# Optimization experiments

Hardware: AMD Instinct MI355X
Metric: run time of the kernel (lower is better)

The kernel has to match this reference:

```python
import jax, jax.numpy as jnp
import numpy as np

EPS = 1e-5  # BatchNorm eps (torch default)

def _bn(x, gamma, beta):
    # training-mode BatchNorm over the edge/node (leading) axis, biased var
    mean = x.mean(axis=0, keepdims=True)
    var = x.var(axis=0, keepdims=True)
    return (x - mean) * jax.lax.rsqrt(var + EPS) * gamma + beta

def _silu(x):
    return x * jax.nn.sigmoid(x)

def setup_inputs() -> dict:
    N, E, H, NH = 50000, 800000, 128, 4
    HD = H // NH
    key = jax.random.key(0)
    ks = jax.random.split(key, 8)
    x = jax.random.normal(ks[0], (N, H), dtype=jnp.float32)
    weight = jax.random.uniform(ks[1], (N, 1), dtype=jnp.float32)  # positive fraction weights
    src = jax.random.randint(ks[2], (E,), 0, N)
    dst = jax.random.randint(ks[3], (E,), 0, N)
    # f: Linear(2H, 1) + BN(1)
    Wf = jax.random.normal(ks[4], (2 * H, 1), dtype=jnp.float32) * 0.05
    bf = jnp.zeros((1,), jnp.float32)
    f_gamma = jnp.ones((1,), jnp.float32)
    f_beta = jnp.zeros((1,), jnp.float32)
    # g: NH heads of Linear(2H, HD) + BN(HD), stacked on leading head axis
    Wg = jax.random.normal(ks[5], (NH, 2 * H, HD), dtype=jnp.float32) * 0.05
    bg = jnp.zeros((NH, HD), jnp.float32)
    g_gamma = jnp.ones((NH, HD), jnp.float32)
    g_beta = jnp.zeros((NH, HD), jnp.float32)
    # bn_nodes: BN(H)
    n_gamma = jnp.ones((H,), jnp.float32)
    n_beta = jnp.zeros((H,), jnp.float32)
    return dict(x=x, weight=weight, src=src, dst=dst, Wf=Wf, bf=bf,
                f_gamma=f_gamma, f_beta=f_beta, Wg=Wg, bg=bg,
                g_gamma=g_gamma, g_beta=g_beta, n_gamma=n_gamma, n_beta=n_beta)

def reference(x, weight, src, dst, Wf, bf, f_gamma, f_beta, Wg, bg, g_gamma, g_beta, n_gamma, n_beta):
    N = x.shape[0]
    E = src.shape[0]
    # per-edge concat of src/dst node features: [E, 2H]
    hihj = jnp.concatenate([x[src], x[dst]], axis=-1)
    # attention logit f(hihj) = SiLU(BN(Linear)) then exp: [E, 1]
    exp_e = jnp.exp(_silu(_bn(hihj @ Wf + bf, f_gamma, f_beta)))
    # weighted softmax-like normalization over incoming edges of each dst node
    we = weight[src] * exp_e                                   # [E, 1]
    sum_w_exp = jax.ops.segment_sum(we, dst, num_segments=N)   # [N, 1]
    a = we / sum_w_exp[dst]                                    # [E, 1]
    # multi-head message: a_ij * SiLU(BN(Linear_h(hihj))) per head, concat
    z = jnp.einsum('ed,hdk->ehk', hihj, Wg) + bg               # [E, NH, HD]
    z = _silu(_bn(z, g_gamma, g_beta))
    msg = (a[:, :, None] * z).reshape(E, -1)                   # [E, H]
    h = jax.ops.segment_sum(msg, dst, num_segments=N)          # [N, H]
    out = _bn(h, n_gamma, n_beta) + x                          # residual
    return out
```

## Files before the change

kernel.cpp:

```cpp
#include <hip/hip_runtime.h>
#include <hip/hip_bf16.h>
#include <math.h>

#define HDIM 128
#define PAD 64
typedef unsigned short ushort_t;
typedef unsigned int uint_t;
typedef __attribute__((ext_vector_type(8))) short bf16x8;
typedef __attribute__((ext_vector_type(4))) float f32x4;
typedef __attribute__((ext_vector_type(2))) float v2f;

__device__ __forceinline__ float wave_allreduce(float v){
  #pragma unroll
  for (int o = 1; o < 64; o <<= 1) v += __shfl_xor(v, o);
  return v;
}

__device__ __forceinline__ ushort_t f2bf(float f){
  uint_t u = __float_as_uint(f);
  uint_t r = (u + 0x7fffu + ((u >> 16) & 1u)) >> 16;
  return (ushort_t)r;
}

__device__ __forceinline__ v2f bf2(uint_t u){
  v2f r;
  r.x = __uint_as_float(u << 16);
  r.y = __uint_as_float(u & 0xffff0000u);
  return r;
}

__global__ __launch_bounds__(128) void k_wpack(const float* __restrict__ Wg,
    const float* __restrict__ Wf, ushort_t* __restrict__ W2t,
    int* __restrict__ cnt, int N){
  int b = blockIdx.x;
  int k = threadIdx.x;
  if (b < 272){
    float val;
    if (b < 128)       val = Wg[(size_t)(b >> 5) * 8192 + k * 32 + (b & 31)];
    else if (b < 256){ int c2 = b - 128;
                       val = Wg[(size_t)(c2 >> 5) * 8192 + (k + 128) * 32 + (c2 & 31)]; }
    else if (b == 256) val = Wf[k];
    else if (b == 257) val = Wf[128 + k];
    else               val = 0.f;
    W2t[(size_t)b * 128 + k] = f2bf(val);
  } else {
    int i = (b - 272) * 128 + k;
    if (i < N) cnt[i] = 0;
  }
}

__global__ __launch_bounds__(256) void k_gemmfill(const float* __restrict__ x,
    const ushort_t* __restrict__ W2t, const float* __restrict__ weight,
    ushort_t* __restrict__ Pb, ushort_t* __restrict__ Qb,
    float* __restrict__ v, float2* __restrict__ uw2,
    const int* __restrict__ src, const int* __restrict__ dst,
    int* __restrict__ cnt, int* __restrict__ es,
    int N, int E, int GB){
  if ((int)blockIdx.x < GB){
    int wid = __builtin_amdgcn_readfirstlane(threadIdx.x >> 6);
    int lane = threadIdx.x & 63;
    int quad = lane >> 4, col = lane & 15;
    int strip = blockIdx.x * 2 + (wid >> 1);
    int half = wid & 1;
    int n_base = strip * 16;
    if (n_base >= N) return;
    int tbeg = half * 8;
    int ntile = half ? 9 : 8;
    f32x4 acc[9];
    #pragma unroll
    for (int t = 0; t < 9; ++t) acc[t] = (f32x4){0.f, 0.f, 0.f, 0.f};
    int row = n_base + col;
    int rowc = row < N ? row : N - 1;
    const float* xr = x + (size_t)rowc * HDIM + quad * 8;
    #pragma unroll
    for (int kk = 0; kk < 4; ++kk){
      float4 a0 = *(const float4*)(xr + kk * 32);
      float4 a1 = *(const float4*)(xr + kk * 32 + 4);
      bf16x8 af;
      af[0] = (short)f2bf(a0.x); af[1] = (short)f2bf(a0.y);
      af[2] = (short)f2bf(a0.z); af[3] = (short)f2bf(a0.w);
      af[4] = (short)f2bf(a1.x); af[5] = (short)f2bf(a1.y);
      af[6] = (short)f2bf(a1.z); af[7] = (short)f2bf(a1.w);
      const ushort_t* wb = W2t + (size_t)(tbeg * 16) * 128 + (size_t)col * 128 + kk * 32 + quad * 8;
      #pragma unroll
      for (int t = 0; t < 9; ++t){
        if (t < ntile){
          bf16x8 bfr = *(const bf16x8*)(wb + (size_t)t * 16 * 128);
          acc[t] = __builtin_amdgcn_mfma_f32_16x16x32_bf16(af, bfr, acc[t], 0, 0, 0);
        }
      }
    }
    #pragma unroll
    for (int t = 0; t < 8; ++t){
      int ct = tbeg + t;
      int c = ct * 16 + col;
      #pragma unroll
      for (int r = 0; r < 4; ++r){
        int n = n_base + quad * 4 + r;
        if (n < N){
          ushort_t valb = f2bf(acc[t][r]);
          if (c < 128) Pb[(size_t)n * HDIM + c] = valb;
          else         Qb[(size_t)n * HDIM + (c - 128)] = valb;
        }
      }
    }
    if (half){
      #pragma unroll
      for (int r = 0; r < 4; ++r){
        int n = n_base + quad * 4 + r;
        if (n < N){
          float val = acc[8][r];
          if (col == 0)      uw2[n] = make_float2(val, weight[n]);
          else if (col == 1) v[n] = val;
        }
      }
    }
  } else {
    int bi = blockIdx.x - GB;
    int part = bi & 7;
    int nch = (gridDim.x - GB) >> 3;
    int chunk = bi >> 3;
    int Npp = (N + 7) >> 3;
    int lo = part * Npp;
    int hi = lo + Npp; if (hi > N) hi = N;
    int stride = nch * 256;
    for (int e = chunk * 256 + threadIdx.x; e < E; e += stride){
      int d = dst[e];
      if (d >= lo && d < hi){
        int c = atomicAdd(&cnt[d], 1);
        if (c < PAD) es[(size_t)d * PAD + c] = src[e];
      }
    }
  }
}

__global__ __launch_bounds__(256) void k_gstats(const ushort_t* __restrict__ Pb,
    const ushort_t* __restrict__ Qb, const float* __restrict__ v,
    const float2* __restrict__ uw2, const int* __restrict__ es,
    const int* __restrict__ cnt, float* __restrict__ pstatG, int N, int NW){
  int lane = threadIdx.x & 63;
  int wid = __builtin_amdgcn_readfirstlane(threadIdx.x >> 6);
  int wg = blockIdx.x * 4 + wid;
  const uint_t* Pu = (const uint_t*)Pb;
  const uint_t* Qu = (const uint_t*)Qb;
  v2f gs = {0.f, 0.f}, gq = {0.f, 0.f};
  float fs = 0.f, fq = 0.f;
  for (int n = wg; n < N; n += NW){
    int dn = cnt[n]; dn = dn < PAD ? dn : PAD;
    v2f q = bf2(Qu[(size_t)n * 64 + lane]);
    float vn = v[n];
    int sj = 0;
    if (lane < dn){
      sj = es[(size_t)n * PAD + lane];
      float t = uw2[sj].x + vn;
      fs += t; fq = fmaf(t, t, fq);
    }
    int j = 0;
    for (; j + 3 < dn; j += 4){
      int s0 = __shfl(sj, j),     s1 = __shfl(sj, j + 1);
      int s2 = __shfl(sj, j + 2), s3 = __shfl(sj, j + 3);
      uint_t p0 = Pu[(size_t)s0 * 64 + lane];
      uint_t p1 = Pu[(size_t)s1 * 64 + lane];
      uint_t p2 = Pu[(size_t)s2 * 64 + lane];
      uint_t p3 = Pu[(size_t)s3 * 64 + lane];
      v2f y0 = bf2(p0) + q, y1 = bf2(p1) + q, y2 = bf2(p2) + q, y3 = bf2(p3) + q;
      gs += y0 + y1 + y2 + y3;
      gq += y0 * y0; gq += y1 * y1; gq += y2 * y2; gq += y3 * y3;
    }
    for (; j < dn; ++j){
      int s0 = __shfl(sj, j);
      v2f y0 = bf2(Pu[(size_t)s0 * 64 + lane]) + q;
      gs += y0; gq += y0 * y0;
    }
  }
  fs = wave_allreduce(fs); fq = wave_allreduce(fq);
  float* pb = pstatG + (size_t)wg * 258;
  *(float2*)&pb[2 * lane]       = make_float2(gs.x, gs.y);
  *(float2*)&pb[128 + 2 * lane] = make_float2(gq.x, gq.y);
  if (lane == 0){ pb[256] = fs; pb[257] = fq; }
}

__global__ __launch_bounds__(256) void k_redfin1(const float* __restrict__ pstatG,
    int NW, const float* __restrict__ g_gamma, const float* __restrict__ g_beta,
    const float* __restrict__ f_gamma, const float* __restrict__ f_beta,
    float* __restrict__ fin, long long E){
  int j = blockIdx.x;
  int c1 = (j < 128) ? j : 256;
  int c2 = (j < 128) ? 128 + j : 257;
  double s1 = 0, s2 = 0;
  for (int b = threadIdx.x; b < NW; b += 256){
    const float* pb = pstatG + (size_t)b * 258;
    s1 += (double)pb[c1]; s2 += (double)pb[c2];
  }
  __shared__ double m1[256], m2[256];
  m1[threadIdx.x] = s1; m2[threadIdx.x] = s2;
  __syncthreads();
  for (int o = 128; o; o >>= 1){
    if (threadIdx.x < o){ m1[threadIdx.x] += m1[threadIdx.x + o];
                          m2[threadIdx.x] += m2[threadIdx.x + o]; }
    __syncthreads();
  }
  if (threadIdx.x == 0){
    double m = m1[0] / (double)E;
    double var = m2[0] / (double)E - m * m;
    if (j < 128){
      float sc = (float)((double)g_gamma[j] / sqrt(var + 1e-5));
      fin[2 + j] = sc; fin[130 + j] = g_beta[j] - (float)m * sc;
    } else {
      float sc = (float)((double)f_gamma[0] / sqrt(var + 1e-5));
      fin[0] = sc; fin[1] = f_beta[0] - (float)m * sc;
    }
  }
}

__global__ __launch_bounds__(256) void k_msg(const ushort_t* __restrict__ Pb,
    const ushort_t* __restrict__ Qb, const float* __restrict__ v,
    const float2* __restrict__ uw2, const int* __restrict__ es,
    const int* __restrict__ cnt, const float* __restrict__ fin,
    float* __restrict__ h, float* __restrict__ pstatH, int N, int NW){
  int lane = threadIdx.x & 63;
  int wid = __builtin_amdgcn_readfirstlane(threadIdx.x >> 6);
  int wg = blockIdx.x * 4 + wid;
  const uint_t* Pu = (const uint_t*)Pb;
  const uint_t* Qu = (const uint_t*)Qb;
  float fsc = fin[0], fsh = fin[1];
  v2f gsc = {fin[2 + 2 * lane], fin[3 + 2 * lane]};
  v2f gsh = {fin[130 + 2 * lane], fin[131 + 2 * lane]};
  v2f hs = {0.f, 0.f}, hq = {0.f, 0.f};
  for (int n = wg; n < N; n += NW){
    int dn = cnt[n]; dn = dn < PAD ? dn : PAD;
    float vn = v[n];
    int sj = 0; float wj = 0.f;
    if (lane < dn){
      sj = es[(size_t)n * PAD + lane];
      float2 uw = uw2[sj];
      float t = fmaf(uw.x + vn, fsc, fsh);
      float sl = t * __builtin_amdgcn_rcpf(1.f + __expf(-t));
      wj = uw.y * __expf(sl);
    }
    float sw = wave_allreduce(wj);
    wj *= (dn > 0) ? (1.f / sw) : 0.f;
    v2f q = bf2(Qu[(size_t)n * 64 + lane]);
    v2f acc = {0.f, 0.f};
    int j = 0;
    for (; j + 3 < dn; j += 4){
      int s0 = __shfl(sj, j),     s1 = __shfl(sj, j + 1);
      int s2 = __shfl(sj, j + 2), s3 = __shfl(sj, j + 3);
      float a0 = __shfl(wj, j),     a1 = __shfl(wj, j + 1);
      float a2 = __shfl(wj, j + 2), a3 = __shfl(wj, j + 3);
      uint_t p0 = Pu[(size_t)s0 * 64 + lane];
      uint_t p1 = Pu[(size_t)s1 * 64 + lane];
      uint_t p2 = Pu[(size_t)s2 * 64 + lane];
      uint_t p3 = Pu[(size_t)s3 * 64 + lane];
      {
        v2f y = (bf2(p0) + q) * gsc + gsh;
        float e0 = __expf(-y.x), e1 = __expf(-y.y);
        float d0 = 1.f + e0, d1 = 1.f + e1;
        float r = __builtin_amdgcn_rcpf(d0 * d1) * a0;
        v2f z; z.x = y.x * d1; z.y = y.y * d0;
        acc += z * (v2f){r, r};
      }
      {
        v2f y = (bf2(p1) + q) * gsc + gsh;
        float e0 = __expf(-y.x), e1 = __expf(-y.y);
        float d0 = 1.f + e0, d1 = 1.f + e1;
        float r = __builtin_amdgcn_rcpf(d0 * d1) * a1;
        v2f z; z.x = y.x * d1; z.y = y.y * d0;
        acc += z * (v2f){r, r};
      }
      {
        v2f y = (bf2(p2) + q) * gsc + gsh;
        float e0 = __expf(-y.x), e1 = __expf(-y.y);
        float d0 = 1.f + e0, d1 = 1.f + e1;
        float r = __builtin_amdgcn_rcpf(d0 * d1) * a2;
        v2f z; z.x = y.x * d1; z.y = y.y * d0;
        acc += z * (v2f){r, r};
      }
      {
        v2f y = (bf2(p3) + q) * gsc + gsh;
        float e0 = __expf(-y.x), e1 = __expf(-y.y);
        float d0 = 1.f + e0, d1 = 1.f + e1;
        float r = __builtin_amdgcn_rcpf(d0 * d1) * a3;
        v2f z; z.x = y.x * d1; z.y = y.y * d0;
        acc += z * (v2f){r, r};
      }
    }
    for (; j < dn; ++j){
      int s0 = __shfl(sj, j);
      float a0 = __shfl(wj, j);
      v2f y = (bf2(Pu[(size_t)s0 * 64 + lane]) + q) * gsc + gsh;
      float e0 = __expf(-y.x), e1 = __expf(-y.y);
      float d0 = 1.f + e0, d1 = 1.f + e1;
      float r = __builtin_amdgcn_rcpf(d0 * d1) * a0;
      v2f z; z.x = y.x * d1; z.y = y.y * d0;
      acc += z * (v2f){r, r};
    }
    *(float2*)&h[(size_t)n * 128 + 2 * lane] = make_float2(acc.x, acc.y);
    hs += acc; hq += acc * acc;
  }
  float* pb = pstatH + (size_t)wg * 256;
  *(float2*)&pb[2 * lane]       = make_float2(hs.x, hs.y);
  *(float2*)&pb[128 + 2 * lane] = make_float2(hq.x, hq.y);
}

__global__ __launch_bounds__(256) void k_redfin2(const float* __restrict__ pstatH,
    int NW, const float* __restrict__ n_gamma, const float* __restrict__ n_beta,
    float* __restrict__ fin, int N){
  int j = blockIdx.x;
  double s1 = 0, s2 = 0;
  for (int b = threadIdx.x; b < NW; b += 256){
    const float* pb = pstatH + (size_t)b * 256;
    s1 += (double)pb[j]; s2 += (double)pb[128 + j];
  }
  __shared__ double m1[256], m2[256];
  m1[threadIdx.x] = s1; m2[threadIdx.x] = s2;
  __syncthreads();
  for (int o = 128; o; o >>= 1){
    if (threadIdx.x < o){ m1[threadIdx.x] += m1[threadIdx.x + o];
                          m2[threadIdx.x] += m2[threadIdx.x + o]; }
    __syncthreads();
  }
  if (threadIdx.x == 0){
    double m = m1[0] / (double)N;
    double var = m2[0] / (double)N - m * m;
    float sc = (float)((double)n_gamma[j] / sqrt(var + 1e-5));
    fin[258 + j] = sc; fin[386 + j] = n_beta[j] - (float)m * sc;
  }
}

__global__ __launch_bounds__(256) void k_out(const float* __restrict__ h,
    const float* __restrict__ x, const float* __restrict__ fin,
    float* __restrict__ out, int total4){
  int i = blockIdx.x * 256 + threadIdx.x;
  if (i >= total4) return;
  const float4* h4 = (const float4*)h; const float4* x4 = (const float4*)x;
  float4 hv = h4[i], xv = x4[i];
  int c = (i * 4) & 127;
  float4 o;
  o.x = fmaf(hv.x, fin[258 + c],     fin[386 + c])     + xv.x;
  o.y = fmaf(hv.y, fin[258 + c + 1], fin[386 + c + 1]) + xv.y;
  o.z = fmaf(hv.z, fin[258 + c + 2], fin[386 + c + 2]) + xv.z;
  o.w = fmaf(hv.w, fin[258 + c + 3], fin[386 + c + 3]) + xv.w;
  ((float4*)out)[i] = o;
}

extern "C" void kernel_launch(void* const* d_in, const int* in_sizes, int n_in,
                              void* d_out, int out_size, void* d_ws, size_t ws_size,
                              hipStream_t stream){
  const float* x       = (const float*)d_in[0];
  const float* weight  = (const float*)d_in[1];
  const int*   src     = (const int*)d_in[2];
  const int*   dst     = (const int*)d_in[3];
  const float* Wf      = (const float*)d_in[4];
  const float* f_gamma = (const float*)d_in[6];
  const float* f_beta  = (const float*)d_in[7];
  const float* Wg      = (const float*)d_in[8];
  const float* g_gamma = (const float*)d_in[10];
  const float* g_beta  = (const float*)d_in[11];
  const float* n_gamma = (const float*)d_in[12];
  const float* n_beta  = (const float*)d_in[13];
  float* out = (float*)d_out;

  int N = in_sizes[0] / HDIM;
  int E = in_sizes[2];

  char* ws = (char*)d_ws;
  size_t off = 0;
  auto alloc = [&](size_t bytes)->char*{
    char* p = ws + off; off = (off + bytes + 255) & ~(size_t)255; return p;
  };
  ushort_t* Pb    = (ushort_t*)alloc((size_t)N * HDIM * 2);
  ushort_t* Qb    = (ushort_t*)alloc((size_t)N * HDIM * 2);
  float* h        = (float*)alloc((size_t)N * HDIM * 4);
  float* v        = (float*)alloc((size_t)N * 4);
  float2* uw2     = (float2*)alloc((size_t)N * 8);
  int* es         = (int*)alloc((size_t)N * PAD * 4);
  ushort_t* W2t   = (ushort_t*)alloc((size_t)272 * 128 * 2);
  int* cnt        = (int*)alloc((size_t)N * 4);
  const int NWB = 2048;
  const int NW  = NWB * 4;
  float*  pstatG = (float*)alloc((size_t)NW * 258 * 4);
  float*  pstatH = (float*)alloc((size_t)NW * 256 * 4);
  float*  fin    = (float*)alloc(514 * 4);

  int GB = (N + 31) / 32;
  const int FB = 4096;

  k_wpack   <<<272 + (N + 127) / 128, 128, 0, stream>>>(Wg, Wf, W2t, cnt, N);
  k_gemmfill<<<GB + FB, 256, 0, stream>>>(x, W2t, weight, Pb, Qb, v, uw2,
                                          src, dst, cnt, es, N, E, GB);
  k_gstats  <<<NWB, 256, 0, stream>>>(Pb, Qb, v, uw2, es, cnt, pstatG, N, NW);
  k_redfin1 <<<129, 256, 0, stream>>>(pstatG, NW, g_gamma, g_beta, f_gamma, f_beta, fin, (long long)E);
  k_msg     <<<NWB, 256, 0, stream>>>(Pb, Qb, v, uw2, es, cnt, fin, h, pstatH, N, NW);
  k_redfin2 <<<128, 256, 0, stream>>>(pstatH, NW, n_gamma, n_beta, fin, N);
  k_out     <<<(N * HDIM / 4 + 255) / 256, 256, 0, stream>>>(h, x, fin, out, N * HDIM / 4);
}
```

Baseline: 302.2 us.

## Fuse stats, reductions, message and output into one cooperative kernel with grid syncs

Replaces the gstats, redfin1, msg, redfin2 and out kernels with a single cooperative kernel that uses grid.sync() between phases, launched with 1024 blocks (down from 2048 waves-blocks), and splits the combined GEMM/fill kernel into two separate launches. The goal is to remove per-launch overhead and the gaps between the small reduction kernels. In exchange it adds grid-wide barrier cost, limits the grid to co-resident blocks, and serializes the GEMM and edge fill instead of running them concurrently in one launch.

```diff
diff --git a/kernel.cpp b/kernel.cpp
--- a/kernel.cpp
+++ b/kernel.cpp
@@ -1,6 +1,9 @@
 #include <hip/hip_runtime.h>
 #include <hip/hip_bf16.h>
+#include <hip/hip_cooperative_groups.h>
 #include <math.h>
+
+namespace cg = cooperative_groups;
 
 #define HDIM 128
 #define PAD 64
@@ -49,299 +52,297 @@
   }
 }
 
-__global__ __launch_bounds__(256) void k_gemmfill(const float* __restrict__ x,
+__global__ __launch_bounds__(256) void k_gemm2(const float* __restrict__ x,
     const ushort_t* __restrict__ W2t, const float* __restrict__ weight,
     ushort_t* __restrict__ Pb, ushort_t* __restrict__ Qb,
-    float* __restrict__ v, float2* __restrict__ uw2,
-    const int* __restrict__ src, const int* __restrict__ dst,
-    int* __restrict__ cnt, int* __restrict__ es,
-    int N, int E, int GB){
-  if ((int)blockIdx.x < GB){
-    int wid = __builtin_amdgcn_readfirstlane(threadIdx.x >> 6);
-    int lane = threadIdx.x & 63;
-    int quad = lane >> 4, col = lane & 15;
-    int strip = blockIdx.x * 2 + (wid >> 1);
-    int half = wid & 1;
-    int n_base = strip * 16;
-    if (n_base >= N) return;
-    int tbeg = half * 8;
-    int ntile = half ? 9 : 8;
-    f32x4 acc[9];
+    float* __restrict__ v, float2* __restrict__ uw2, int N){
+  int wid = __builtin_amdgcn_readfirstlane(threadIdx.x >> 6);
+  int lane = threadIdx.x & 63;
+  int quad = lane >> 4, col = lane & 15;
+  int strip = blockIdx.x * 2 + (wid >> 1);
+  int half = wid & 1;
+  int n_base = strip * 16;
+  if (n_base >= N) return;
+  int tbeg = half * 8;
+  int ntile = half ? 9 : 8;
+  f32x4 acc[9];
+  #pragma unroll
+  for (int t = 0; t < 9; ++t) acc[t] = (f32x4){0.f, 0.f, 0.f, 0.f};
+  int row = n_base + col;
+  int rowc = row < N ? row : N - 1;
+  const float* xr = x + (size_t)rowc * HDIM + quad * 8;
+  #pragma unroll
+  for (int kk = 0; kk < 4; ++kk){
+    float4 a0 = *(const float4*)(xr + kk * 32);
+    float4 a1 = *(const float4*)(xr + kk * 32 + 4);
+    bf16x8 af;
+    af[0] = (short)f2bf(a0.x); af[1] = (short)f2bf(a0.y);
+    af[2] = (short)f2bf(a0.z); af[3] = (short)f2bf(a0.w);
+    af[4] = (short)f2bf(a1.x); af[5] = (short)f2bf(a1.y);
+    af[6] = (short)f2bf(a1.z); af[7] = (short)f2bf(a1.w);
+    const ushort_t* wb = W2t + (size_t)(tbeg * 16) * 128 + (size_t)col * 128 + kk * 32 + quad * 8;
     #pragma unroll
-    for (int t = 0; t < 9; ++t) acc[t] = (f32x4){0.f, 0.f, 0.f, 0.f};
-    int row = n_base + col;
-    int rowc = row < N ? row : N - 1;
-    const float* xr = x + (size_t)rowc * HDIM + quad * 8;
+    for (int t = 0; t < 9; ++t){
+      if (t < ntile){
+        bf16x8 bfr = *(const bf16x8*)(wb + (size_t)t * 16 * 128);
+        acc[t] = __builtin_amdgcn_mfma_f32_16x16x32_bf16(af, bfr, acc[t], 0, 0, 0);
+      }
+    }
+  }
+  #pragma unroll
+  for (int t = 0; t < 8; ++t){
+    int ct = tbeg + t;
+    int c = ct * 16 + col;
     #pragma unroll
-    for (int kk = 0; kk < 4; ++kk){
-      float4 a0 = *(const float4*)(xr + kk * 32);
-      float4 a1 = *(const float4*)(xr + kk * 32 + 4);
-      bf16x8 af;
-      af[0] = (short)f2bf(a0.x); af[1] = (short)f2bf(a0.y);
-      af[2] = (short)f2bf(a0.z); af[3] = (short)f2bf(a0.w);
-      af[4] = (short)f2bf(a1.x); af[5] = (short)f2bf(a1.y);
-      af[6] = (short)f2bf(a1.z); af[7] = (short)f2bf(a1.w);
-      const ushort_t* wb = W2t + (size_t)(tbeg * 16) * 128 + (size_t)col * 128 + kk * 32 + quad * 8;
-      #pragma unroll
-      for (int t = 0; t < 9; ++t){
-        if (t < ntile){
-          bf16x8 bfr = *(const bf16x8*)(wb + (size_t)t * 16 * 128);
-          acc[t] = __builtin_amdgcn_mfma_f32_16x16x32_bf16(af, bfr, acc[t], 0, 0, 0);
-        }
-      }
-    }
+    for (int r = 0; r < 4; ++r){
+      int n = n_base + quad * 4 + r;
+      if (n < N){
+        ushort_t valb = f2bf(acc[t][r]);
+        if (c < 128) Pb[(size_t)n * HDIM + c] = valb;
+        else         Qb[(size_t)n * HDIM + (c - 128)] = valb;
+      }
+    }
+  }
+  if (half){
     #pragma unroll
-    for (int t = 0; t < 8; ++t){
-      int ct = tbeg + t;
-      int c = ct * 16 + col;
-      #pragma unroll
-      for (int r = 0; r < 4; ++r){
-        int n = n_base + quad * 4 + r;
-        if (n < N){
-          ushort_t valb = f2bf(acc[t][r]);
-          if (c < 128) Pb[(size_t)n * HDIM + c] = valb;
-          else         Qb[(size_t)n * HDIM + (c - 128)] = valb;
-        }
-      }
-    }
-    if (half){
-      #pragma unroll
-      for (int r = 0; r < 4; ++r){
-        int n = n_base + quad * 4 + r;
-        if (n < N){
-          float val = acc[8][r];
-          if (col == 0)      uw2[n] = make_float2(val, weight[n]);
-          else if (col == 1) v[n] = val;
-        }
-      }
-    }
-  } else {
-    int bi = blockIdx.x - GB;
-    int part = bi & 7;
-    int nch = (gridDim.x - GB) >> 3;
-    int chunk = bi >> 3;
-    int Npp = (N + 7) >> 3;
-    int lo = part * Npp;
-    int hi = lo + Npp; if (hi > N) hi = N;
-    int stride = nch * 256;
-    for (int e = chunk * 256 + threadIdx.x; e < E; e += stride){
-      int d = dst[e];
-      if (d >= lo && d < hi){
-        int c = atomicAdd(&cnt[d], 1);
-        if (c < PAD) es[(size_t)d * PAD + c] = src[e];
-      }
-    }
-  }
-}
-
-__global__ __launch_bounds__(256) void k_gstats(const ushort_t* __restrict__ Pb,
-    const ushort_t* __restrict__ Qb, const float* __restrict__ v,
-    const float2* __restrict__ uw2, const int* __restrict__ es,
-    const int* __restrict__ cnt, float* __restrict__ pstatG, int N, int NW){
+    for (int r = 0; r < 4; ++r){
+      int n = n_base + quad * 4 + r;
+      if (n < N){
+        float val = acc[8][r];
+        if (col == 0)      uw2[n] = make_float2(val, weight[n]);
+        else if (col == 1) v[n] = val;
+      }
+    }
+  }
+}
+
+__global__ __launch_bounds__(256) void k_fillx(const int* __restrict__ src,
+    const int* __restrict__ dst, int* __restrict__ cnt, int* __restrict__ es,
+    int E, int N){
+  int part = blockIdx.x & 7;
+  int nch = gridDim.x >> 3;
+  int chunk = blockIdx.x >> 3;
+  int Npp = (N + 7) >> 3;
+  int lo = part * Npp;
+  int hi = lo + Npp; if (hi > N) hi = N;
+  int stride = nch * 256;
+  for (int e = chunk * 256 + threadIdx.x; e < E; e += stride){
+    int d = dst[e];
+    if (d >= lo && d < hi){
+      int c = atomicAdd(&cnt[d], 1);
+      if (c < PAD) es[(size_t)d * PAD + c] = src[e];
+    }
+  }
+}
+
+__global__ __launch_bounds__(256, 4) void k_mega(
+    const ushort_t* __restrict__ Pb, const ushort_t* __restrict__ Qb,
+    const float* __restrict__ v, const float2* __restrict__ uw2,
+    const int* __restrict__ es, const int* __restrict__ cnt,
+    const float* __restrict__ g_gamma, const float* __restrict__ g_beta,
+    const float* __restrict__ f_gamma, const float* __restrict__ f_beta,
+    const float* __restrict__ n_gamma, const float* __restrict__ n_beta,
+    const float* __restrict__ x, float* __restrict__ out,
+    float* __restrict__ pstatG, float* __restrict__ pstatH,
+    float* __restrict__ fin, float* __restrict__ h,
+    int N, long long E){
+  cg::grid_group grid = cg::this_grid();
+  __shared__ double m1[256], m2[256];
   int lane = threadIdx.x & 63;
   int wid = __builtin_amdgcn_readfirstlane(threadIdx.x >> 6);
+  int NW = gridDim.x * 4;
   int wg = blockIdx.x * 4 + wid;
   const uint_t* Pu = (const uint_t*)Pb;
   const uint_t* Qu = (const uint_t*)Qb;
-  v2f gs = {0.f, 0.f}, gq = {0.f, 0.f};
-  float fs = 0.f, fq = 0.f;
-  for (int n = wg; n < N; n += NW){
-    int dn = cnt[n]; dn = dn < PAD ? dn : PAD;
-    v2f q = bf2(Qu[(size_t)n * 64 + lane]);
-    float vn = v[n];
-    int sj = 0;
-    if (lane < dn){
-      sj = es[(size_t)n * PAD + lane];
-      float t = uw2[sj].x + vn;
-      fs += t; fq = fmaf(t, t, fq);
-    }
-    int j = 0;
-    for (; j + 3 < dn; j += 4){
-      int s0 = __shfl(sj, j),     s1 = __shfl(sj, j + 1);
-      int s2 = __shfl(sj, j + 2), s3 = __shfl(sj, j + 3);
-      uint_t p0 = Pu[(size_t)s0 * 64 + lane];
-      uint_t p1 = Pu[(size_t)s1 * 64 + lane];
-      uint_t p2 = Pu[(size_t)s2 * 64 + lane];
-      uint_t p3 = Pu[(size_t)s3 * 64 + lane];
-      v2f y0 = bf2(p0) + q, y1 = bf2(p1) + q, y2 = bf2(p2) + q, y3 = bf2(p3) + q;
-      gs += y0 + y1 + y2 + y3;
-      gq += y0 * y0; gq += y1 * y1; gq += y2 * y2; gq += y3 * y3;
-    }
-    for (; j < dn; ++j){
-      int s0 = __shfl(sj, j);
-      v2f y0 = bf2(Pu[(size_t)s0 * 64 + lane]) + q;
-      gs += y0; gq += y0 * y0;
-    }
-  }
-  fs = wave_allreduce(fs); fq = wave_allreduce(fq);
-  float* pb = pstatG + (size_t)wg * 258;
-  *(float2*)&pb[2 * lane]       = make_float2(gs.x, gs.y);
-  *(float2*)&pb[128 + 2 * lane] = make_float2(gq.x, gq.y);
-  if (lane == 0){ pb[256] = fs; pb[257] = fq; }
-}
-
-__global__ __launch_bounds__(256) void k_redfin1(const float* __restrict__ pstatG,
-    int NW, const float* __restrict__ g_gamma, const float* __restrict__ g_beta,
-    const float* __restrict__ f_gamma, const float* __restrict__ f_beta,
-    float* __restrict__ fin, long long E){
-  int j = blockIdx.x;
-  int c1 = (j < 128) ? j : 256;
-  int c2 = (j < 128) ? 128 + j : 257;
-  double s1 = 0, s2 = 0;
-  for (int b = threadIdx.x; b < NW; b += 256){
-    const float* pb = pstatG + (size_t)b * 258;
-    s1 += (double)pb[c1]; s2 += (double)pb[c2];
-  }
-  __shared__ double m1[256], m2[256];
-  m1[threadIdx.x] = s1; m2[threadIdx.x] = s2;
-  __syncthreads();
-  for (int o = 128; o; o >>= 1){
-    if (threadIdx.x < o){ m1[threadIdx.x] += m1[threadIdx.x + o];
-                          m2[threadIdx.x] += m2[threadIdx.x + o]; }
+
+  {
+    v2f gs = {0.f, 0.f}, gq = {0.f, 0.f};
+    float fs = 0.f, fq = 0.f;
+    for (int n = wg; n < N; n += NW){
+      int dn = cnt[n]; dn = dn < PAD ? dn : PAD;
+      v2f q = bf2(Qu[(size_t)n * 64 + lane]);
+      float vn = v[n];
+      int sj = 0;
+      if (lane < dn){
+        sj = es[(size_t)n * PAD + lane];
+        float t = uw2[sj].x + vn;
+        fs += t; fq = fmaf(t, t, fq);
+      }
+      int j = 0;
+      for (; j + 3 < dn; j += 4){
+        int s0 = __shfl(sj, j),     s1 = __shfl(sj, j + 1);
+        int s2 = __shfl(sj, j + 2), s3 = __shfl(sj, j + 3);
+        uint_t p0 = Pu[(size_t)s0 * 64 + lane];
+        uint_t p1 = Pu[(size_t)s1 * 64 + lane];
+        uint_t p2 = Pu[(size_t)s2 * 64 + lane];
+        uint_t p3 = Pu[(size_t)s3 * 64 + lane];
+        v2f y0 = bf2(p0) + q, y1 = bf2(p1) + q, y2 = bf2(p2) + q, y3 = bf2(p3) + q;
+        gs += y0 + y1 + y2 + y3;
+        gq += y0 * y0; gq += y1 * y1; gq += y2 * y2; gq += y3 * y3;
+      }
+      for (; j < dn; ++j){
+        int s0 = __shfl(sj, j);
+        v2f y0 = bf2(Pu[(size_t)s0 * 64 + lane]) + q;
+        gs += y0; gq += y0 * y0;
+      }
+    }
+    fs = wave_allreduce(fs); fq = wave_allreduce(fq);
+    float* pb = pstatG + (size_t)wg * 258;
+    *(float2*)&pb[2 * lane]       = make_float2(gs.x, gs.y);
+    *(float2*)&pb[128 + 2 * lane] = make_float2(gq.x, gq.y);
+    if (lane == 0){ pb[256] = fs; pb[257] = fq; }
+  }
+  grid.sync();
+
+  if (blockIdx.x < 129){
+    int j = blockIdx.x;
+    int c1 = (j < 128) ? j : 256;
+    int c2 = (j < 128) ? 128 + j : 257;
+    double s1 = 0, s2 = 0;
+    for (int b = threadIdx.x; b < NW; b += 256){
+      const float* pb = pstatG + (size_t)b * 258;
+      s1 += (double)pb[c1]; s2 += (double)pb[c2];
+    }
+    m1[threadIdx.x] = s1; m2[threadIdx.x] = s2;
     __syncthreads();
-  }
-  if (threadIdx.x == 0){
-    double m = m1[0] / (double)E;
-    double var = m2[0] / (double)E - m * m;
-    if (j < 128){
-      float sc = (float)((double)g_gamma[j] / sqrt(var + 1e-5));
-      fin[2 + j] = sc; fin[130 + j] = g_beta[j] - (float)m * sc;
-    } else {
-      float sc = (float)((double)f_gamma[0] / sqrt(var + 1e-5));
-      fin[0] = sc; fin[1] = f_beta[0] - (float)m * sc;
-    }
-  }
-}
-
-__global__ __launch_bounds__(256) void k_msg(const ushort_t* __restrict__ Pb,
-    const ushort_t* __restrict__ Qb, const float* __restrict__ v,
-    const float2* __restrict__ uw2, const int* __restrict__ es,
-    const int* __restrict__ cnt, const float* __restrict__ fin,
-    float* __restrict__ h, float* __restrict__ pstatH, int N, int NW){
-  int lane = threadIdx.x & 63;
-  int wid = __builtin_amdgcn_readfirstlane(threadIdx.x >> 6);
-  int wg = blockIdx.x * 4 + wid;
-  const uint_t* Pu = (const uint_t*)Pb;
-  const uint_t* Qu = (const uint_t*)Qb;
-  float fsc = fin[0], fsh = fin[1];
-  v2f gsc = {fin[2 + 2 * lane], fin[3 + 2 * lane]};
-  v2f gsh = {fin[130 + 2 * lane], fin[131 + 2 * lane]};
-  v2f hs = {0.f, 0.f}, hq = {0.f, 0.f};
-  for (int n = wg; n < N; n += NW){
-    int dn = cnt[n]; dn = dn < PAD ? dn : PAD;
-    float vn = v[n];
-    int sj = 0; float wj = 0.f;
-    if (lane < dn){
-      sj = es[(size_t)n * PAD + lane];
-      float2 uw = uw2[sj];
-      float t = fmaf(uw.x + vn, fsc, fsh);
-      float sl = t * __builtin_amdgcn_rcpf(1.f + __expf(-t));
-      wj = uw.y * __expf(sl);
-    }
-    float sw = wave_allreduce(wj);
-    wj *= (dn > 0) ? (1.f / sw) : 0.f;
-    v2f q = bf2(Qu[(size_t)n * 64 + lane]);
-    v2f acc = {0.f, 0.f};
-    int j = 0;
-    for (; j + 3 < dn; j += 4){
-      int s0 = __shfl(sj, j),     s1 = __shfl(sj, j + 1);
-      int s2 = __shfl(sj, j + 2), s3 = __shfl(sj, j + 3);
-      float a0 = __shfl(wj, j),     a1 = __shfl(wj, j + 1);
-      float a2 = __shfl(wj, j + 2), a3 = __shfl(wj, j + 3);
-      uint_t p0 = Pu[(size_t)s0 * 64 + lane];
-      uint_t p1 = Pu[(size_t)s1 * 64 + lane];
-      uint_t p2 = Pu[(size_t)s2 * 64 + lane];
-      uint_t p3 = Pu[(size_t)s3 * 64 + lane];
-      {
-        v2f y = (bf2(p0) + q) * gsc + gsh;
+    for (int o = 128; o; o >>= 1){
+      if (threadIdx.x < o){ m1[threadIdx.x] += m1[threadIdx.x + o];
+                            m2[threadIdx.x] += m2[threadIdx.x + o]; }
+      __syncthreads();
+    }
+    if (threadIdx.x == 0){
+      double m = m1[0] / (double)E;
+      double var = m2[0] / (double)E - m * m;
+      if (j < 128){
+        float sc = (float)((double)g_gamma[j] / sqrt(var + 1e-5));
+        fin[2 + j] = sc; fin[130 + j] = g_beta[j] - (float)m * sc;
+      } else {
+        float sc = (float)((double)f_gamma[0] / sqrt(var + 1e-5));
+        fin[0] = sc; fin[1] = f_beta[0] - (float)m * sc;
+      }
+    }
+  }
+  grid.sync();
+
+  {
+    float fsc = fin[0], fsh = fin[1];
+    v2f gsc = {fin[2 + 2 * lane], fin[3 + 2 * lane]};
+    v2f gsh = {fin[130 + 2 * lane], fin[131 + 2 * lane]};
+    v2f hs = {0.f, 0.f}, hq = {0.f, 0.f};
+    for (int n = wg; n < N; n += NW){
+      int dn = cnt[n]; dn = dn < PAD ? dn : PAD;
+      float vn = v[n];
+      int sj = 0; float wj = 0.f;
+      if (lane < dn){
+        sj = es[(size_t)n * PAD + lane];
+        float2 uw = uw2[sj];
+        float t = fmaf(uw.x + vn, fsc, fsh);
+        float sl = t * __builtin_amdgcn_rcpf(1.f + __expf(-t));
+        wj = uw.y * __expf(sl);
+      }
+      float sw = wave_allreduce(wj);
+      wj *= (dn > 0) ? (1.f / sw) : 0.f;
+      v2f q = bf2(Qu[(size_t)n * 64 + lane]);
+      v2f acc = {0.f, 0.f};
+      int j = 0;
+      for (; j + 3 < dn; j += 4){
+        int s0 = __shfl(sj, j),     s1 = __shfl(sj, j + 1);
+        int s2 = __shfl(sj, j + 2), s3 = __shfl(sj, j + 3);
+        float a0 = __shfl(wj, j),     a1 = __shfl(wj, j + 1);
+        float a2 = __shfl(wj, j + 2), a3 = __shfl(wj, j + 3);
+        uint_t p0 = Pu[(size_t)s0 * 64 + lane];
+        uint_t p1 = Pu[(size_t)s1 * 64 + lane];
+        uint_t p2 = Pu[(size_t)s2 * 64 + lane];
+        uint_t p3 = Pu[(size_t)s3 * 64 + lane];
+        {
+          v2f y = (bf2(p0) + q) * gsc + gsh;
+          float e0 = __expf(-y.x), e1 = __expf(-y.y);
+          float d0 = 1.f + e0, d1 = 1.f + e1;
+          float r = __builtin_amdgcn_rcpf(d0 * d1) * a0;
+          v2f z; z.x = y.x * d1; z.y = y.y * d0;
+          acc += z * (v2f){r, r};
+        }
+        {
+          v2f y = (bf2(p1) + q) * gsc + gsh;
+          float e0 = __expf(-y.x), e1 = __expf(-y.y);
+          float d0 = 1.f + e0, d1 = 1.f + e1;
+          float r = __builtin_amdgcn_rcpf(d0 * d1) * a1;
+          v2f z; z.x = y.x * d1; z.y = y.y * d0;
+          acc += z * (v2f){r, r};
+        }
+        {
+          v2f y = (bf2(p2) + q) * gsc + gsh;
+          float e0 = __expf(-y.x), e1 = __expf(-y.y);
+          float d0 = 1.f + e0, d1 = 1.f + e1;
+          float r = __builtin_amdgcn_rcpf(d0 * d1) * a2;
+          v2f z; z.x = y.x * d1; z.y = y.y * d0;
+          acc += z * (v2f){r, r};
+        }
+        {
+          v2f y = (bf2(p3) + q) * gsc + gsh;
+          float e0 = __expf(-y.x), e1 = __expf(-y.y);
+          float d0 = 1.f + e0, d1 = 1.f + e1;
+          float r = __builtin_amdgcn_rcpf(d0 * d1) * a3;
+          v2f z; z.x = y.x * d1; z.y = y.y * d0;
+          acc += z * (v2f){r, r};
+        }
+      }
+      for (; j < dn; ++j){
+        int s0 = __shfl(sj, j);
+        float a0 = __shfl(wj, j);
+        v2f y = (bf2(Pu[(size_t)s0 * 64 + lane]) + q) * gsc + gsh;
         float e0 = __expf(-y.x), e1 = __expf(-y.y);
         float d0 = 1.f + e0, d1 = 1.f + e1;
         float r = __builtin_amdgcn_rcpf(d0 * d1) * a0;
         v2f z; z.x = y.x * d1; z.y = y.y * d0;
         acc += z * (v2f){r, r};
       }
-      {
-        v2f y = (bf2(p1) + q) * gsc + gsh;
-        float e0 = __expf(-y.x), e1 = __expf(-y.y);
-        float d0 = 1.f + e0, d1 = 1.f + e1;
-        float r = __builtin_amdgcn_rcpf(d0 * d1) * a1;
-        v2f z; z.x = y.x * d1; z.y = y.y * d0;
-        acc += z * (v2f){r, r};
-      }
-      {
-        v2f y = (bf2(p2) + q) * gsc + gsh;
-        float e0 = __expf(-y.x), e1 = __expf(-y.y);
-        float d0 = 1.f + e0, d1 = 1.f + e1;
-        float r = __builtin_amdgcn_rcpf(d0 * d1) * a2;
-        v2f z; z.x = y.x * d1; z.y = y.y * d0;
-        acc += z * (v2f){r, r};
-      }
-      {
-        v2f y = (bf2(p3) + q) * gsc + gsh;
-        float e0 = __expf(-y.x), e1 = __expf(-y.y);
-        float d0 = 1.f + e0, d1 = 1.f + e1;
-        float r = __builtin_amdgcn_rcpf(d0 * d1) * a3;
-        v2f z; z.x = y.x * d1; z.y = y.y * d0;
-        acc += z * (v2f){r, r};
-      }
-    }
-    for (; j < dn; ++j){
-      int s0 = __shfl(sj, j);
-      float a0 = __shfl(wj, j);
-      v2f y = (bf2(Pu[(size_t)s0 * 64 + lane]) + q) * gsc + gsh;
-      float e0 = __expf(-y.x), e1 = __expf(-y.y);
-      float d0 = 1.f + e0, d1 = 1.f + e1;
-      float r = __builtin_amdgcn_rcpf(d0 * d1) * a0;
-      v2f z; z.x = y.x * d1; z.y = y.y * d0;
-      acc += z * (v2f){r, r};
-    }
-    *(float2*)&h[(size_t)n * 128 + 2 * lane] = make_float2(acc.x, acc.y);
-    hs += acc; hq += acc * acc;
-  }
-  float* pb = pstatH + (size_t)wg * 256;
-  *(float2*)&pb[2 * lane]       = make_float2(hs.x, hs.y);
-  *(float2*)&pb[128 + 2 * lane] = make_float2(hq.x, hq.y);
-}
-
-__global__ __launch_bounds__(256) void k_redfin2(const float* __restrict__ pstatH,
-    int NW, const float* __restrict__ n_gamma, const float* __restrict__ n_beta,
-    float* __restrict__ fin, int N){
-  int j = blockIdx.x;
-  double s1 = 0, s2 = 0;
-  for (int b = threadIdx.x; b < NW; b += 256){
-    const float* pb = pstatH + (size_t)b * 256;
-    s1 += (double)pb[j]; s2 += (double)pb[128 + j];
-  }
-  __shared__ double m1[256], m2[256];
-  m1[threadIdx.x] = s1; m2[threadIdx.x] = s2;
-  __syncthreads();
-  for (int o = 128; o; o >>= 1){
-    if (threadIdx.x < o){ m1[threadIdx.x] += m1[threadIdx.x + o];
-                          m2[threadIdx.x] += m2[threadIdx.x + o]; }
+      *(float2*)&h[(size_t)n * 128 + 2 * lane] = make_float2(acc.x, acc.y);
+      hs += acc; hq += acc * acc;
+    }
+    float* pb = pstatH + (size_t)wg * 256;
+    *(float2*)&pb[2 * lane]       = make_float2(hs.x, hs.y);
+    *(float2*)&pb[128 + 2 * lane] = make_float2(hq.x, hq.y);
+  }
+  grid.sync();
+
+  if (blockIdx.x < 128){
+    int j = blockIdx.x;
+    double s1 = 0, s2 = 0;
+    for (int b = threadIdx.x; b < NW; b += 256){
+      const float* pb = pstatH + (size_t)b * 256;
+      s1 += (double)pb[j]; s2 += (double)pb[128 + j];
+    }
+    m1[threadIdx.x] = s1; m2[threadIdx.x] = s2;
     __syncthreads();
-  }
-  if (threadIdx.x == 0){
-    double m = m1[0] / (double)N;
-    double var = m2[0] / (double)N - m * m;
-    float sc = (float)((double)n_gamma[j] / sqrt(var + 1e-5));
-    fin[258 + j] = sc; fin[386 + j] = n_beta[j] - (float)m * sc;
-  }
-}
-
-__global__ __launch_bounds__(256) void k_out(const float* __restrict__ h,
-    const float* __restrict__ x, const float* __restrict__ fin,
-    float* __restrict__ out, int total4){
-  int i = blockIdx.x * 256 + threadIdx.x;
-  if (i >= total4) return;
-  const float4* h4 = (const float4*)h; const float4* x4 = (const float4*)x;
-  float4 hv = h4[i], xv = x4[i];
-  int c = (i * 4) & 127;
-  float4 o;
-  o.x = fmaf(hv.x, fin[258 + c],     fin[386 + c])     + xv.x;
-  o.y = fmaf(hv.y, fin[258 + c + 1], fin[386 + c + 1]) + xv.y;
-  o.z = fmaf(hv.z, fin[258 + c + 2], fin[386 + c + 2]) + xv.z;
-  o.w = fmaf(hv.w, fin[258 + c + 3], fin[386 + c + 3]) + xv.w;
-  ((float4*)out)[i] = o;
+    for (int o = 128; o; o >>= 1){
+      if (threadIdx.x < o){ m1[threadIdx.x] += m1[threadIdx.x + o];
+                            m2[threadIdx.x] += m2[threadIdx.x + o]; }
+      __syncthreads();
+    }
+    if (threadIdx.x == 0){
+      double m = m1[0] / (double)N;
+      double var = m2[0] / (double)N - m * m;
+      float sc = (float)((double)n_gamma[j] / sqrt(var + 1e-5));
+      fin[258 + j] = sc; fin[386 + j] = n_beta[j] - (float)m * sc;
+    }
+  }
+  grid.sync();
+
+  {
+    int total4 = N * (HDIM / 4);
+    const float4* h4 = (const float4*)h; const float4* x4 = (const float4*)x;
+    for (int i = blockIdx.x * 256 + threadIdx.x; i < total4; i += gridDim.x * 256){
+      float4 hv = h4[i], xv = x4[i];
+      int c = (i * 4) & 127;
+      float4 o;
+      o.x = fmaf(hv.x, fin[258 + c],     fin[386 + c])     + xv.x;
+      o.y = fmaf(hv.y, fin[258 + c + 1], fin[386 + c + 1]) + xv.y;
+      o.z = fmaf(hv.z, fin[258 + c + 2], fin[386 + c + 2]) + xv.z;
+      o.w = fmaf(hv.w, fin[258 + c + 3], fin[386 + c + 3]) + xv.w;
+      ((float4*)out)[i] = o;
+    }
+  }
 }
 
 extern "C" void kernel_launch(void* const* d_in, const int* in_sizes, int n_in,
@@ -377,21 +378,23 @@
   int* es         = (int*)alloc((size_t)N * PAD * 4);
   ushort_t* W2t   = (ushort_t*)alloc((size_t)272 * 128 * 2);
   int* cnt        = (int*)alloc((size_t)N * 4);
-  const int NWB = 2048;
-  const int NW  = NWB * 4;
+  const int MB = 1024;
+  const int NW = MB * 4;
   float*  pstatG = (float*)alloc((size_t)NW * 258 * 4);
   float*  pstatH = (float*)alloc((size_t)NW * 256 * 4);
   float*  fin    = (float*)alloc(514 * 4);
 
-  int GB = (N + 31) / 32;
-  const int FB = 4096;
-
-  k_wpack   <<<272 + (N + 127) / 128, 128, 0, stream>>>(Wg, Wf, W2t, cnt, N);
-  k_gemmfill<<<GB + FB, 256, 0, stream>>>(x, W2t, weight, Pb, Qb, v, uw2,
-                                          src, dst, cnt, es, N, E, GB);
-  k_gstats  <<<NWB, 256, 0, stream>>>(Pb, Qb, v, uw2, es, cnt, pstatG, N, NW);
-  k_redfin1 <<<129, 256, 0, stream>>>(pstatG, NW, g_gamma, g_beta, f_gamma, f_beta, fin, (long long)E);
-  k_msg     <<<NWB, 256, 0, stream>>>(Pb, Qb, v, uw2, es, cnt, fin, h, pstatH, N, NW);
-  k_redfin2 <<<128, 256, 0, stream>>>(pstatH, NW, n_gamma, n_beta, fin, N);
-  k_out     <<<(N * HDIM / 4 + 255) / 256, 256, 0, stream>>>(h, x, fin, out, N * HDIM / 4);
-}
+  k_wpack <<<272 + (N + 127) / 128, 128, 0, stream>>>(Wg, Wf, W2t, cnt, N);
+  k_gemm2 <<<(N + 31) / 32, 256, 0, stream>>>(x, W2t, weight, Pb, Qb, v, uw2, N);
+  k_fillx <<<8 * 1024, 256, 0, stream>>>(src, dst, cnt, es, E, N);
+
+  long long El = (long long)E;
+  void* args[] = {
+    (void*)&Pb, (void*)&Qb, (void*)&v, (void*)&uw2, (void*)&es, (void*)&cnt,
+    (void*)&g_gamma, (void*)&g_beta, (void*)&f_gamma, (void*)&f_beta,
+    (void*)&n_gamma, (void*)&n_beta, (void*)&x, (void*)&out,
+    (void*)&pstatG, (void*)&pstatH, (void*)&fin, (void*)&h,
+    (void*)&N, (void*)&El
+  };
+  hipLaunchCooperativeKernel((void*)k_mega, dim3(MB), dim3(256), args, 0, stream);
+}
```

Result: slower. 791.5 us (+161.9%).
